# Performance work log

Measured on AMD Instinct MI355X. Metric: run time of the kernel, lower is better.

## Reference

```python
import jax, jax.numpy as jnp
import numpy as np
from jax.scipy.special import logsumexp

DIM_N, DIM_E, DIM_U = 64, 128, 64
MID, A = 32, 16
N_PER, B = 12, 128  # 128 fully-connected graphs of 12 nodes


def _lin_params(k, fin, fout):
    k1, k2 = jax.random.split(k)
    lim = 1.0 / np.sqrt(fin)
    W = jax.random.uniform(k1, (fin, fout), minval=-lim, maxval=lim)
    b = jax.random.uniform(k2, (fout,), minval=-lim, maxval=lim)
    return W, b


def setup_inputs() -> dict:
    key = jax.random.key(0)
    ks = jax.random.split(key, 12)
    # fully connected directed graph (no self loops), per component
    s, d = np.meshgrid(np.arange(N_PER), np.arange(N_PER), indexing='ij')
    m = s != d
    s1, d1 = s[m].astype(np.int64), d[m].astype(np.int64)
    Epg = s1.size  # 132
    M = np.zeros((N_PER, N_PER), np.int64)
    M[s1, d1] = np.arange(Epg)
    rev1 = M[d1, s1]
    noff = (np.arange(B, dtype=np.int64) * N_PER)[:, None]
    eoff = (np.arange(B, dtype=np.int64) * Epg)[:, None]
    src = jnp.asarray((s1[None] + noff).reshape(-1))
    dst = jnp.asarray((d1[None] + noff).reshape(-1))
    idx_revs = jnp.asarray((rev1[None] + eoff).reshape(-1))
    E, Nt = B * Epg, B * N_PER
    edge_feats = jax.random.normal(ks[0], (E, DIM_E))
    node_feats = jax.random.normal(ks[1], (Nt, DIM_N))
    graph_feats = jax.random.normal(ks[2], (B, DIM_U))
    edge_feat_reflected = edge_feats[idx_revs]
    u = jax.random.uniform(ks[3], (E, 2), minval=1e-6, maxval=1.0)
    gumbel_noise = -jnp.log(-jnp.log(u))
    W_jf, b_jf = _lin_params(ks[4], DIM_E + DIM_U, A * MID)
    W_if, b_if = _lin_params(ks[5], DIM_N + DIM_U, A)
    W_ju, b_ju = _lin_params(ks[6], DIM_E + DIM_U, A * MID)
    W_iu, b_iu = _lin_params(ks[7], DIM_N + DIM_U, A)
    W_fl, b_fl = _lin_params(ks[8], DIM_E + DIM_U, MID)
    W_cls, b_cls = _lin_params(ks[9], MID, 2)
    return dict(edge_feats=edge_feats, node_feats=node_feats, graph_feats=graph_feats,
                edge_feat_reflected=edge_feat_reflected, src=src, dst=dst, idx_revs=idx_revs,
                gumbel_noise=gumbel_noise, W_jf=W_jf, b_jf=b_jf, W_if=W_if, b_if=b_if,
                W_ju=W_ju, b_ju=b_ju, W_iu=W_iu, b_iu=b_iu, W_fl=W_fl, b_fl=b_fl,
                W_cls=W_cls, b_cls=b_cls)


def reference(edge_feats, node_feats, graph_feats, edge_feat_reflected, src, dst, idx_revs,
              gumbel_noise, W_jf, b_jf, W_if, b_if, W_ju, b_ju, W_iu, b_iu,
              W_fl, b_fl, W_cls, b_cls):
    Bn = graph_feats.shape[0]
    Nt = node_feats.shape[0]
    E = edge_feats.shape[0]
    npg = Nt // Bn          # nodes per graph == number of BP iterations
    epg = E // Bn
    a = b_if.shape[0]       # num_acts
    mid = W_cls.shape[0]    # mid_pair

    # broadcast graph-level features to edges / nodes
    u_e = jnp.repeat(graph_feats, epg, axis=0)   # [E, du]
    u_n = jnp.repeat(graph_feats, npg, axis=0)   # [Nt, du]

    xe = jnp.concatenate([edge_feats, u_e], axis=-1)
    xer = jnp.concatenate([edge_feat_reflected, u_e], axis=-1)
    xn = jnp.concatenate([node_feats, u_n], axis=-1)

    indiv_factor = xn @ W_if + b_if      # [Nt, A]
    indiv_util = xn @ W_iu + b_iu        # [Nt, A]

    fc = (xe @ W_jf + b_jf).reshape(E, a, mid)
    fcr = (xer @ W_jf + b_jf).reshape(E, a, mid)
    factor_vals = jnp.einsum('eam,ebm->eab', fc, fcr)   # [E, A, A]
    uc = (xe @ W_ju + b_ju).reshape(E, a, mid)
    ucr = (xer @ W_ju + b_ju).reshape(E, a, mid)
    util_vals = jnp.einsum('eam,ebm->eab', uc, ucr)     # [E, A, A]

    # hard gumbel-softmax edge gating; noise shared with reverse edge
    flag_repr = (xe @ W_fl + b_fl) * (xer @ W_fl + b_fl)
    logits = flag_repr @ W_cls + b_cls                  # [E, 2]
    eid = jnp.arange(E)
    noise = gumbel_noise[jnp.minimum(eid, idx_revs)]
    y_soft = jax.nn.softmax(logits + noise, axis=-1)
    y_hard = jax.nn.one_hot(jnp.argmax(y_soft, axis=-1), 2, dtype=y_soft.dtype)
    flags = y_soft + jax.lax.stop_gradient(y_hard - y_soft)
    flag0 = flags[:, 0][:, None]                        # [E, 1]

    fvT = factor_vals.transpose(0, 2, 1)
    uvT = util_vals.transpose(0, 2, 1)
    if_src, if_dst = indiv_factor[src], indiv_factor[dst]
    iu_src, iu_dst = indiv_util[src], indiv_util[dst]

    def step(carry, _):
        mm_n, um_n, msg_e, rmsg_e, umsg_e, rumsg_e = carry
        agg = mm_n[src] - rmsg_e + if_src                      # [E, A]
        m = factor_vals + agg[:, None, :]                      # [E, A, A]
        m_sum = jax.nn.log_softmax(logsumexp(m, axis=-1), axis=-1)
        new_msg = m_sum * flag0
        agg_rev = mm_n[dst] - msg_e + if_dst
        m_rev = fvT + agg_rev[:, None, :]
        m_rev_sum = jax.nn.log_softmax(logsumexp(m_rev, axis=-1), axis=-1)
        new_rmsg = m_rev_sum * flag0
        util = um_n[src] - rumsg_e + iu_src
        new_umsg = ((util_vals + util[:, None, :]) * jax.nn.softmax(m, axis=-1)).sum(-1) * flag0
        rev_util = um_n[dst] - umsg_e + iu_dst
        new_rumsg = ((uvT + rev_util[:, None, :]) * jax.nn.softmax(m_rev, axis=-1)).sum(-1) * flag0
        new_mm_n = jax.ops.segment_sum(new_msg, dst, num_segments=Nt)
        new_um_n = jax.ops.segment_sum(new_umsg, dst, num_segments=Nt)
        return (new_mm_n, new_um_n, new_msg, new_rmsg, new_umsg, new_rumsg), None

    zn = jnp.zeros((Nt, a), edge_feats.dtype)
    ze = jnp.zeros((E, a), edge_feats.dtype)
    carry0 = (zn, zn, ze, ze, ze, ze)
    (mm_n, um_n, _, _, _, _), _ = jax.lax.scan(step, carry0, None, length=npg)

    node0 = jnp.arange(Bn) * npg
    return (um_n + indiv_util)[node0]   # [B, A]
```

## Files before the change

kernel.cpp:

```cpp
#include <hip/hip_runtime.h>
#include <hip/hip_bf16.h>

typedef unsigned short ushort_t;
typedef __bf16 bf16x8 __attribute__((ext_vector_type(8)));
typedef float f32x4 __attribute__((ext_vector_type(4)));

#define E_TOT 16896
#define NT    1536
#define BGR   128
#define NPG   12
#define EPG   132
#define KD    192
#define KD2   576
#define NJ    512
#define ADIM  16
#define MIDD  32
#define NCAN  8448

#if defined(__has_builtin)
#  if __has_builtin(__builtin_amdgcn_global_load_lds)
#    define HAS_GLL 1
#  else
#    define HAS_GLL 0
#  endif
#else
#  define HAS_GLL 0
#endif

#if HAS_GLL
__device__ __forceinline__ void gll16(const ushort_t* g, ushort_t* s) {
    __builtin_amdgcn_global_load_lds(
        (const __attribute__((address_space(1))) unsigned int*)g,
        (__attribute__((address_space(3))) unsigned int*)s, 16, 0, 0);
}
#endif

__device__ __forceinline__ float b2f(ushort_t u) {
    union { float f; unsigned int i; } c; c.i = ((unsigned int)u) << 16; return c.f;
}
__device__ __forceinline__ ushort_t f2b(float f) {
    union { float f; unsigned int i; } c; c.f = f;
    unsigned int i = c.i;
    unsigned int r = (i + 0x7FFFu + ((i >> 16) & 1u)) >> 16;
    return (ushort_t)r;
}
__device__ __forceinline__ int rev_local(int i) {
    int s = i / 11;
    int p = i - 11 * s;
    int d = p + (p >= s ? 1 : 0);
    return d * 11 + (s < d ? s : s - 1);
}

__global__ __launch_bounds__(256) void prep_kernel(
    const float* __restrict__ Wjf, const float* __restrict__ Wju,
    const float* __restrict__ ef,  const float* __restrict__ gf,
    ushort_t* __restrict__ WtJFs, ushort_t* __restrict__ WtJUs,
    ushort_t* __restrict__ XeS)
{
    int idx = blockIdx.x * 256 + threadIdx.x;
    const int T1 = NJ * KD;
    if (idx < T1) {
        int n = idx / KD, k = idx - n * KD;
        float wf = Wjf[k * NJ + n];
        ushort_t hf = f2b(wf);
        WtJFs[n * KD2 + k]       = hf;
        WtJFs[n * KD2 + 192 + k] = hf;
        WtJFs[n * KD2 + 384 + k] = f2b(wf - b2f(hf));
        float wu = Wju[k * NJ + n];
        ushort_t hu = f2b(wu);
        WtJUs[n * KD2 + k]       = hu;
        WtJUs[n * KD2 + 192 + k] = hu;
        WtJUs[n * KD2 + 384 + k] = f2b(wu - b2f(hu));
        return;
    }
    idx -= T1;
    if (idx < E_TOT * KD) {
        int e = idx / KD, k = idx - e * KD;
        float x = (k < 128) ? ef[(size_t)e * 128 + k] : gf[(e / EPG) * 64 + (k - 128)];
        ushort_t h = f2b(x);
        XeS[(size_t)e * KD2 + k]       = h;
        XeS[(size_t)e * KD2 + 192 + k] = f2b(x - b2f(h));
        XeS[(size_t)e * KD2 + 384 + k] = h;
    }
}

__global__ __launch_bounds__(256) void gemm_kernel(
    const ushort_t* __restrict__ X,
    const ushort_t* __restrict__ Wt0, const ushort_t* __restrict__ Wt1,
    const float* __restrict__ b0, const float* __restrict__ b1,
    float* __restrict__ Hbase)
{
    __shared__ ushort_t As[2][128][32];
    __shared__ ushort_t Bs[2][128][32];
    int z = blockIdx.z;
    const ushort_t* Wt = z ? Wt1 : Wt0;
    const float* bias = z ? b1 : b0;
    float* H = Hbase + (size_t)z * E_TOT * NJ;

    int tid = threadIdx.x, lane = tid & 63, w = tid >> 6;
    int m0 = blockIdx.y * 128, n0 = blockIdx.x * 128;
    int wm = (w >> 1) * 64, wn = (w & 1) * 64;
    int r = lane & 15, q = lane >> 4;
    f32x4 acc[4][4] = {};

    int sr = w * 32 + (lane >> 2);
    int sc = (lane & 3) * 8;
    const ushort_t* xg0 = X  + (size_t)(m0 + sr)      * KD2 + sc;
    const ushort_t* xg1 = X  + (size_t)(m0 + sr + 16) * KD2 + sc;
    const ushort_t* wg0 = Wt + (size_t)(n0 + sr)      * KD2 + sc;
    const ushort_t* wg1 = Wt + (size_t)(n0 + sr + 16) * KD2 + sc;

#if HAS_GLL
    auto stage = [&](int p, int kk) {
        gll16(xg0 + kk, &As[p][w * 32][0]);
        gll16(xg1 + kk, &As[p][w * 32 + 16][0]);
        gll16(wg0 + kk, &Bs[p][w * 32][0]);
        gll16(wg1 + kk, &Bs[p][w * 32 + 16][0]);
    };
#else
    auto stage = [&](int p, int kk) {
        uint4 a0 = *(const uint4*)(xg0 + kk);
        uint4 a1 = *(const uint4*)(xg1 + kk);
        uint4 bb0 = *(const uint4*)(wg0 + kk);
        uint4 bb1 = *(const uint4*)(wg1 + kk);
        *(uint4*)&As[p][sr][sc]      = a0;
        *(uint4*)&As[p][sr + 16][sc] = a1;
        *(uint4*)&Bs[p][sr][sc]      = bb0;
        *(uint4*)&Bs[p][sr + 16][sc] = bb1;
    };
#endif

    stage(0, 0);
    int cur = 0;
    for (int kk = 0; kk < KD2; kk += 32) {
        __syncthreads();
        if (kk + 32 < KD2) stage(cur ^ 1, kk + 32);
        bf16x8 af[4], bf[4];
#pragma unroll
        for (int mi = 0; mi < 4; ++mi)
            af[mi] = *(const bf16x8*)&As[cur][wm + mi * 16 + r][q * 8];
#pragma unroll
        for (int ni = 0; ni < 4; ++ni)
            bf[ni] = *(const bf16x8*)&Bs[cur][wn + ni * 16 + r][q * 8];
#pragma unroll
        for (int mi = 0; mi < 4; ++mi)
#pragma unroll
            for (int ni = 0; ni < 4; ++ni)
                acc[mi][ni] = __builtin_amdgcn_mfma_f32_16x16x32_bf16(
                    af[mi], bf[ni], acc[mi][ni], 0, 0, 0);
        cur ^= 1;
    }
#pragma unroll
    for (int ni = 0; ni < 4; ++ni) {
        int col = n0 + wn + ni * 16 + r;
        float bvf = bias[col];
#pragma unroll
        for (int mi = 0; mi < 4; ++mi) {
            int rowb = m0 + wm + mi * 16 + q * 4;
            float* dst = H + (size_t)rowb * NJ + col;
#pragma unroll
            for (int rr = 0; rr < 4; ++rr)
                dst[(size_t)rr * NJ] = acc[mi][ni][rr] + bvf;
        }
    }
}

__global__ __launch_bounds__(256) void pair_kernel(
    const float* __restrict__ Hbase, float* __restrict__ Obase)
{
    __shared__ float sA[4][16][36];
    __shared__ float sB[4][16][36];
    __shared__ float sC[4][16][20];
    const float* H = Hbase + (size_t)blockIdx.y * E_TOT * NJ;
    float* OutV = Obase + (size_t)blockIdx.y * E_TOT * 256;
    int tid = threadIdx.x, w = tid >> 6, lane = tid & 63;
    int c = blockIdx.x * 4 + w;
    int gg = c / 66, cl = c - gg * 66;
    int s = 0;
    while (cl >= 11 - s) { cl -= 11 - s; ++s; }
    int d = s + 1 + cl;
    int e  = gg * EPG + s * 11 + (d - 1);
    int re = gg * EPG + d * 11 + s;
    const float* hA = H + (size_t)e * NJ;
    const float* hB = H + (size_t)re * NJ;
    int a = lane >> 2, mseg = (lane & 3) * 8;
    float4 va0 = *(const float4*)(hA + a * 32 + mseg);
    float4 va1 = *(const float4*)(hA + a * 32 + mseg + 4);
    float4 vb0 = *(const float4*)(hB + a * 32 + mseg);
    float4 vb1 = *(const float4*)(hB + a * 32 + mseg + 4);
    *(float4*)&sA[w][a][mseg]     = va0;
    *(float4*)&sA[w][a][mseg + 4] = va1;
    *(float4*)&sB[w][a][mseg]     = vb0;
    *(float4*)&sB[w][a][mseg + 4] = vb1;
    __syncthreads();

    int b = lane & 15, a0 = (lane >> 4) * 4;
    float4 ac0 = {0,0,0,0}, ac1 = {0,0,0,0}, ac2 = {0,0,0,0}, ac3 = {0,0,0,0};
#pragma unroll
    for (int m4 = 0; m4 < 8; ++m4) {
        float4 vb = *(const float4*)&sB[w][b][m4 * 4];
        float4 x0 = *(const float4*)&sA[w][a0 + 0][m4 * 4];
        float4 x1 = *(const float4*)&sA[w][a0 + 1][m4 * 4];
        float4 x2 = *(const float4*)&sA[w][a0 + 2][m4 * 4];
        float4 x3 = *(const float4*)&sA[w][a0 + 3][m4 * 4];
        ac0.x += x0.x * vb.x; ac0.y += x0.y * vb.y; ac0.z += x0.z * vb.z; ac0.w += x0.w * vb.w;
        ac1.x += x1.x * vb.x; ac1.y += x1.y * vb.y; ac1.z += x1.z * vb.z; ac1.w += x1.w * vb.w;
        ac2.x += x2.x * vb.x; ac2.y += x2.y * vb.y; ac2.z += x2.z * vb.z; ac2.w += x2.w * vb.w;
        ac3.x += x3.x * vb.x; ac3.y += x3.y * vb.y; ac3.z += x3.z * vb.z; ac3.w += x3.w * vb.w;
    }
    float v0 = ac0.x + ac0.y + ac0.z + ac0.w;
    float v1 = ac1.x + ac1.y + ac1.z + ac1.w;
    float v2 = ac2.x + ac2.y + ac2.z + ac2.w;
    float v3 = ac3.x + ac3.y + ac3.z + ac3.w;
    float* oe = OutV + (size_t)e * 256;
    oe[(a0 + 0) * 16 + b] = v0;
    oe[(a0 + 1) * 16 + b] = v1;
    oe[(a0 + 2) * 16 + b] = v2;
    oe[(a0 + 3) * 16 + b] = v3;
    sC[w][b][a0 + 0] = v0;
    sC[w][b][a0 + 1] = v1;
    sC[w][b][a0 + 2] = v2;
    sC[w][b][a0 + 3] = v3;
    __syncthreads();
    int rr = lane >> 2, cc = (lane & 3) * 4;
    float4 t4 = { sC[w][rr][cc], sC[w][rr][cc + 1], sC[w][rr][cc + 2], sC[w][rr][cc + 3] };
    *(float4*)(OutV + (size_t)re * 256 + lane * 4) = t4;
}

__global__ __launch_bounds__(256) void hfl_kernel(
    const float* __restrict__ ef, const float* __restrict__ gf,
    const float* __restrict__ Wfl, const float* __restrict__ bfl,
    float* __restrict__ HFL)
{
    __shared__ float Ws[KD][32];
    __shared__ float xr[64][KD];
    int tid = threadIdx.x;
    int e0 = blockIdx.x * 64;
    for (int i = tid; i < KD * 32; i += 256) Ws[i >> 5][i & 31] = Wfl[i];
    for (int i4 = tid; i4 < 64 * 48; i4 += 256) {
        int slot = i4 / 48, kq = i4 - slot * 48;
        int e = e0 + slot;
        float4 v;
        if (kq < 32) v = *(const float4*)&ef[(size_t)e * 128 + kq * 4];
        else         v = *(const float4*)&gf[(e / EPG) * 64 + (kq - 32) * 4];
        *(float4*)&xr[slot][kq * 4] = v;
    }
    __syncthreads();
    int j = tid & 31, es = tid >> 5;
    float acc[8];
#pragma unroll
    for (int i = 0; i < 8; ++i) acc[i] = bfl[j];
    for (int k = 0; k < KD; k += 4) {
        float w0 = Ws[k][j], w1 = Ws[k + 1][j], w2 = Ws[k + 2][j], w3 = Ws[k + 3][j];
#pragma unroll
        for (int i = 0; i < 8; ++i) {
            float4 x4 = *(const float4*)&xr[es + 8 * i][k];
            acc[i] += x4.x * w0; acc[i] += x4.y * w1;
            acc[i] += x4.z * w2; acc[i] += x4.w * w3;
        }
    }
#pragma unroll
    for (int i = 0; i < 8; ++i)
        HFL[(size_t)(e0 + es + 8 * i) * 32 + j] = acc[i];
}

__global__ __launch_bounds__(704, 3) void bp_kernel(
    const float* __restrict__ FV, const float* __restrict__ UV,
    const float* __restrict__ HFL, const float* __restrict__ Wcls,
    const float* __restrict__ bcls, const float* __restrict__ gum,
    const float* __restrict__ nf, const float* __restrict__ gf,
    const float* __restrict__ Wif, const float* __restrict__ bif,
    const float* __restrict__ Wiu, const float* __restrict__ biu,
    float* __restrict__ out)
{
    int g = blockIdx.x, tid = threadIdx.x;
    __shared__ float msg[2][EPG][16];
    __shared__ float umsg[2][EPG][16];
    __shared__ float Asum[NPG][16], Usum[NPG][16];
    __shared__ float iffs[NPG][16], iuus[NPG][16];
    __shared__ float fls[EPG];

    for (int i = tid; i < 2 * EPG * 16; i += 704) {
        (&msg[0][0][0])[i] = 0.f;
        (&umsg[0][0][0])[i] = 0.f;
    }
    if (tid < NPG * 16) {
        int nl = tid >> 4, aa = tid & 15;
        int n = g * NPG + nl;
        float accf = bif[aa], accu = biu[aa];
        for (int k = 0; k < 128; ++k) {
            float x = (k < 64) ? nf[(size_t)n * 64 + k] : gf[g * 64 + (k - 64)];
            accf += x * Wif[k * 16 + aa];
            accu += x * Wiu[k * 16 + aa];
        }
        iffs[nl][aa] = accf; iuus[nl][aa] = accu;
        Asum[nl][aa] = accf; Usum[nl][aa] = accu;
    }
    if (tid < EPG) {
        int el = tid, rel = rev_local(el);
        int e = g * EPG + el, re = g * EPG + rel;
        float l0 = bcls[0], l1 = bcls[1];
        const float* ha = HFL + (size_t)e * 32;
        const float* hb = HFL + (size_t)re * 32;
#pragma unroll
        for (int j = 0; j < 32; ++j) {
            float p = ha[j] * hb[j];
            l0 += p * Wcls[j * 2 + 0];
            l1 += p * Wcls[j * 2 + 1];
        }
        int mn = min(e, re);
        l0 += gum[(size_t)mn * 2 + 0];
        l1 += gum[(size_t)mn * 2 + 1];
        fls[el] = (l0 >= l1) ? 1.0f : 0.0f;
    }

    int w44 = tid >> 4, a = tid & 15;
    int sidx[3], ridx[3], eidx[3];
    float fv[3][16], uv[3][16], fle[3];
    const float* fvg = FV + (size_t)g * EPG * 256;
    const float* uvg = UV + (size_t)g * EPG * 256;
#pragma unroll
    for (int j = 0; j < 3; ++j) {
        int e = j * 44 + w44;
        eidx[j] = e;
        sidx[j] = e / 11;
        ridx[j] = rev_local(e);
        const float* fr = fvg + (size_t)e * 256 + a * 16;
        const float* ur = uvg + (size_t)e * 256 + a * 16;
#pragma unroll
        for (int q = 0; q < 4; ++q) {
            float4 f4 = *(const float4*)(fr + q * 4);
            float4 u4 = *(const float4*)(ur + q * 4);
            fv[j][q * 4 + 0] = f4.x; fv[j][q * 4 + 1] = f4.y;
            fv[j][q * 4 + 2] = f4.z; fv[j][q * 4 + 3] = f4.w;
            uv[j][q * 4 + 0] = u4.x; uv[j][q * 4 + 1] = u4.y;
            uv[j][q * 4 + 2] = u4.z; uv[j][q * 4 + 3] = u4.w;
        }
    }
    __syncthreads();
#pragma unroll
    for (int j = 0; j < 3; ++j) fle[j] = fls[eidx[j]];

    int cur = 0;
    for (int it = 0; it < NPG; ++it) {
        int nxt = cur ^ 1;
#pragma unroll
        for (int j = 0; j < 3; ++j) {
            int e = eidx[j], s = sidx[j], re = ridx[j];
            float t_m[16], t_u[16];
#pragma unroll
            for (int q = 0; q < 4; ++q) {
                float4 av  = *(const float4*)&Asum[s][q * 4];
                float4 mv  = *(const float4*)&msg[cur][re][q * 4];
                float4 usv = *(const float4*)&Usum[s][q * 4];
                float4 umv = *(const float4*)&umsg[cur][re][q * 4];
                t_m[q * 4 + 0] = fv[j][q * 4 + 0] + (av.x - mv.x);
                t_m[q * 4 + 1] = fv[j][q * 4 + 1] + (av.y - mv.y);
                t_m[q * 4 + 2] = fv[j][q * 4 + 2] + (av.z - mv.z);
                t_m[q * 4 + 3] = fv[j][q * 4 + 3] + (av.w - mv.w);
                t_u[q * 4 + 0] = uv[j][q * 4 + 0] + (usv.x - umv.x);
                t_u[q * 4 + 1] = uv[j][q * 4 + 1] + (usv.y - umv.y);
                t_u[q * 4 + 2] = uv[j][q * 4 + 2] + (usv.z - umv.z);
                t_u[q * 4 + 3] = uv[j][q * 4 + 3] + (usv.w - umv.w);
            }
            float mx = t_m[0];
#pragma unroll
            for (int b = 1; b < 16; ++b) mx = fmaxf(mx, t_m[b]);
            float S = 0.f, num = 0.f;
#pragma unroll
            for (int b = 0; b < 16; ++b) {
                float ev = __expf(t_m[b] - mx);
                S += ev;
                num += t_u[b] * ev;
            }
            float lse = mx + __logf(S);
            float unv = num / S;
            float M2 = lse;
            M2 = fmaxf(M2, __shfl_xor(M2, 1));
            M2 = fmaxf(M2, __shfl_xor(M2, 2));
            M2 = fmaxf(M2, __shfl_xor(M2, 4));
            M2 = fmaxf(M2, __shfl_xor(M2, 8));
            float se = __expf(lse - M2);
            se += __shfl_xor(se, 1);
            se += __shfl_xor(se, 2);
            se += __shfl_xor(se, 4);
            se += __shfl_xor(se, 8);
            float LSE = M2 + __logf(se);
            msg[nxt][e][a] = (lse - LSE) * fle[j];
            umsg[nxt][e][a] = unv * fle[j];
        }
        __syncthreads();
        if (tid < NPG * 16) {
            int n = tid >> 4, aa = tid & 15;
            float sm = 0.f, su = 0.f;
#pragma unroll
            for (int s = 0; s < NPG; ++s) {
                if (s == n) continue;
                int le = s * 11 + (n < s ? n : n - 1);
                sm += msg[nxt][le][aa];
                su += umsg[nxt][le][aa];
            }
            Asum[n][aa] = sm + iffs[n][aa];
            Usum[n][aa] = su + iuus[n][aa];
        }
        __syncthreads();
        cur = nxt;
    }
    if (tid < 16) {
        out[g * 16 + tid] = Usum[0][tid];
    }
}

extern "C" void kernel_launch(void* const* d_in, const int* in_sizes, int n_in,
                              void* d_out, int out_size, void* d_ws, size_t ws_size,
                              hipStream_t stream) {
    const float* edge_feats  = (const float*)d_in[0];
    const float* node_feats  = (const float*)d_in[1];
    const float* graph_feats = (const float*)d_in[2];
    const float* gumbel      = (const float*)d_in[7];
    const float* W_jf        = (const float*)d_in[8];
    const float* b_jf        = (const float*)d_in[9];
    const float* W_if        = (const float*)d_in[10];
    const float* b_if        = (const float*)d_in[11];
    const float* W_ju        = (const float*)d_in[12];
    const float* b_ju        = (const float*)d_in[13];
    const float* W_iu        = (const float*)d_in[14];
    const float* b_iu        = (const float*)d_in[15];
    const float* W_fl        = (const float*)d_in[16];
    const float* b_fl        = (const float*)d_in[17];
    const float* W_cls       = (const float*)d_in[18];
    const float* b_cls       = (const float*)d_in[19];
    float* out = (float*)d_out;
    (void)in_sizes; (void)n_in; (void)out_size;

    size_t off = 0;
    char* base = (char*)d_ws;
    auto alloc = [&](size_t bytes) {
        void* p = base + off;
        off += (bytes + 255) & ~(size_t)255;
        return p;
    };
    ushort_t* XeS   = (ushort_t*)alloc((size_t)E_TOT * KD2 * 2);
    ushort_t* WtJFs = (ushort_t*)alloc((size_t)NJ * KD2 * 2);
    ushort_t* WtJUs = (ushort_t*)alloc((size_t)NJ * KD2 * 2);
    float*    HFL   = (float*)   alloc((size_t)E_TOT * 32 * 4);

    const size_t fused_need = off + (size_t)E_TOT * NJ * 2 * 4
                                  + (size_t)E_TOT * 512 * 4
                                  + 4096;
    const int prep_blocks = (NJ * KD + E_TOT * KD) / 256;

    prep_kernel<<<prep_blocks, 256, 0, stream>>>(W_jf, W_ju, edge_feats, graph_feats,
                                                 WtJFs, WtJUs, XeS);
    hfl_kernel<<<E_TOT / 64, 256, 0, stream>>>(edge_feats, graph_feats, W_fl, b_fl, HFL);

    if (ws_size >= fused_need) {
        float* H2   = (float*)alloc((size_t)E_TOT * NJ * 2 * 4);
        float* FVUV = (float*)alloc((size_t)E_TOT * 512 * 4);
        float* FVv = FVUV;
        float* UVv = FVUV + (size_t)E_TOT * 256;
        gemm_kernel<<<dim3(NJ / 128, E_TOT / 128, 2), 256, 0, stream>>>(
            XeS, WtJFs, WtJUs, b_jf, b_ju, H2);
        pair_kernel<<<dim3(NCAN / 4, 2), 256, 0, stream>>>(H2, FVUV);
        bp_kernel<<<BGR, 704, 0, stream>>>(FVv, UVv, HFL, W_cls, b_cls, gumbel,
                                           node_feats, graph_feats,
                                           W_if, b_if, W_iu, b_iu, out);
    } else {
        float* Hbuf = (float*)alloc((size_t)E_TOT * NJ * 4);
        float* FVv  = (float*)alloc((size_t)E_TOT * 256 * 4);
        float* UVv  = (float*)XeS;
        gemm_kernel<<<dim3(NJ / 128, E_TOT / 128, 1), 256, 0, stream>>>(
            XeS, WtJFs, WtJFs, b_jf, b_jf, Hbuf);
        pair_kernel<<<dim3(NCAN / 4, 1), 256, 0, stream>>>(Hbuf, FVv);
        gemm_kernel<<<dim3(NJ / 128, E_TOT / 128, 1), 256, 0, stream>>>(
            XeS, WtJUs, WtJUs, b_ju, b_ju, Hbuf);
        pair_kernel<<<dim3(NCAN / 4, 1), 256, 0, stream>>>(Hbuf, UVv);
        bp_kernel<<<BGR, 704, 0, stream>>>(FVv, UVv, HFL, W_cls, b_cls, gumbel,
                                           node_feats, graph_feats,
                                           W_if, b_if, W_iu, b_iu, out);
    }
}
```

Baseline: 240.7 us.

## Share A tile across both weight GEMMs and precompute node linears in prep

The GEMM kernel now computes both the factor and utility projections in a single block. It stages one X tile against two weight tiles and keeps two accumulator sets, so X is read from memory once instead of twice. The per-node individual factor/utility linear layers move out of the serial bp_kernel preamble into extra prep_kernel blocks that use shared-memory weights. The low-workspace fallback path is removed. Doubling the accumulators raises register and LDS pressure in the GEMM, which may lower occupancy.

```diff
diff --git a/kernel.cpp b/kernel.cpp
--- a/kernel.cpp
+++ b/kernel.cpp
@@ -13,8 +13,6 @@
 #define KD    192
 #define KD2   576
 #define NJ    512
-#define ADIM  16
-#define MIDD  32
 #define NCAN  8448
 
 #if defined(__has_builtin)
@@ -54,34 +52,61 @@
 __global__ __launch_bounds__(256) void prep_kernel(
     const float* __restrict__ Wjf, const float* __restrict__ Wju,
     const float* __restrict__ ef,  const float* __restrict__ gf,
+    const float* __restrict__ nf,
+    const float* __restrict__ Wif, const float* __restrict__ bif,
+    const float* __restrict__ Wiu, const float* __restrict__ biu,
     ushort_t* __restrict__ WtJFs, ushort_t* __restrict__ WtJUs,
-    ushort_t* __restrict__ XeS)
+    ushort_t* __restrict__ XeS,
+    float* __restrict__ IFF, float* __restrict__ IUU)
 {
-    int idx = blockIdx.x * 256 + threadIdx.x;
+    __shared__ float Ws[128 * 32];
+    __shared__ float xr[8][128];
     const int T1 = NJ * KD;
-    if (idx < T1) {
-        int n = idx / KD, k = idx - n * KD;
-        float wf = Wjf[k * NJ + n];
-        ushort_t hf = f2b(wf);
-        WtJFs[n * KD2 + k]       = hf;
-        WtJFs[n * KD2 + 192 + k] = hf;
-        WtJFs[n * KD2 + 384 + k] = f2b(wf - b2f(hf));
-        float wu = Wju[k * NJ + n];
-        ushort_t hu = f2b(wu);
-        WtJUs[n * KD2 + k]       = hu;
-        WtJUs[n * KD2 + 192 + k] = hu;
-        WtJUs[n * KD2 + 384 + k] = f2b(wu - b2f(hu));
-        return;
-    }
-    idx -= T1;
-    if (idx < E_TOT * KD) {
+    const int NBE = (T1 + E_TOT * KD) / 256;
+    if (blockIdx.x < (unsigned)NBE) {
+        int idx = blockIdx.x * 256 + threadIdx.x;
+        if (idx < T1) {
+            int n = idx / KD, k = idx - n * KD;
+            float wf = Wjf[k * NJ + n];
+            ushort_t hf = f2b(wf);
+            WtJFs[n * KD2 + k]       = hf;
+            WtJFs[n * KD2 + 192 + k] = hf;
+            WtJFs[n * KD2 + 384 + k] = f2b(wf - b2f(hf));
+            float wu = Wju[k * NJ + n];
+            ushort_t hu = f2b(wu);
+            WtJUs[n * KD2 + k]       = hu;
+            WtJUs[n * KD2 + 192 + k] = hu;
+            WtJUs[n * KD2 + 384 + k] = f2b(wu - b2f(hu));
+            return;
+        }
+        idx -= T1;
         int e = idx / KD, k = idx - e * KD;
         float x = (k < 128) ? ef[(size_t)e * 128 + k] : gf[(e / EPG) * 64 + (k - 128)];
         ushort_t h = f2b(x);
         XeS[(size_t)e * KD2 + k]       = h;
         XeS[(size_t)e * KD2 + 192 + k] = f2b(x - b2f(h));
         XeS[(size_t)e * KD2 + 384 + k] = h;
-    }
+        return;
+    }
+    int tid = threadIdx.x;
+    int n0 = (blockIdx.x - NBE) * 8;
+    for (int i = tid; i < 128 * 32; i += 256) {
+        int k = i >> 5, j = i & 31;
+        Ws[i] = (j < 16) ? Wif[k * 16 + j] : Wiu[k * 16 + (j - 16)];
+    }
+    for (int i = tid; i < 8 * 128; i += 256) {
+        int slot = i >> 7, k = i & 127;
+        int n = n0 + slot;
+        xr[slot][k] = (k < 64) ? nf[(size_t)n * 64 + k] : gf[(n / NPG) * 64 + (k - 64)];
+    }
+    __syncthreads();
+    int slot = tid >> 5, j = tid & 31;
+    float acc = (j < 16) ? bif[j] : biu[j - 16];
+#pragma unroll 8
+    for (int k = 0; k < 128; ++k) acc += xr[slot][k] * Ws[k * 32 + j];
+    int n = n0 + slot;
+    if (j < 16) IFF[n * 16 + j] = acc;
+    else        IUU[n * 16 + (j - 16)] = acc;
 }
 
 __global__ __launch_bounds__(256) void gemm_kernel(
@@ -91,42 +116,45 @@
     float* __restrict__ Hbase)
 {
     __shared__ ushort_t As[2][128][32];
-    __shared__ ushort_t Bs[2][128][32];
-    int z = blockIdx.z;
-    const ushort_t* Wt = z ? Wt1 : Wt0;
-    const float* bias = z ? b1 : b0;
-    float* H = Hbase + (size_t)z * E_TOT * NJ;
-
+    __shared__ ushort_t Bs[2][2][128][32];
     int tid = threadIdx.x, lane = tid & 63, w = tid >> 6;
     int m0 = blockIdx.y * 128, n0 = blockIdx.x * 128;
     int wm = (w >> 1) * 64, wn = (w & 1) * 64;
     int r = lane & 15, q = lane >> 4;
-    f32x4 acc[4][4] = {};
+    f32x4 acc[2][4][4] = {};
 
     int sr = w * 32 + (lane >> 2);
     int sc = (lane & 3) * 8;
-    const ushort_t* xg0 = X  + (size_t)(m0 + sr)      * KD2 + sc;
-    const ushort_t* xg1 = X  + (size_t)(m0 + sr + 16) * KD2 + sc;
-    const ushort_t* wg0 = Wt + (size_t)(n0 + sr)      * KD2 + sc;
-    const ushort_t* wg1 = Wt + (size_t)(n0 + sr + 16) * KD2 + sc;
+    const ushort_t* xg0 = X   + (size_t)(m0 + sr)      * KD2 + sc;
+    const ushort_t* xg1 = X   + (size_t)(m0 + sr + 16) * KD2 + sc;
+    const ushort_t* w0g0 = Wt0 + (size_t)(n0 + sr)      * KD2 + sc;
+    const ushort_t* w0g1 = Wt0 + (size_t)(n0 + sr + 16) * KD2 + sc;
+    const ushort_t* w1g0 = Wt1 + (size_t)(n0 + sr)      * KD2 + sc;
+    const ushort_t* w1g1 = Wt1 + (size_t)(n0 + sr + 16) * KD2 + sc;
 
 #if HAS_GLL
     auto stage = [&](int p, int kk) {
-        gll16(xg0 + kk, &As[p][w * 32][0]);
-        gll16(xg1 + kk, &As[p][w * 32 + 16][0]);
-        gll16(wg0 + kk, &Bs[p][w * 32][0]);
-        gll16(wg1 + kk, &Bs[p][w * 32 + 16][0]);
+        gll16(xg0 + kk,  &As[p][w * 32][0]);
+        gll16(xg1 + kk,  &As[p][w * 32 + 16][0]);
+        gll16(w0g0 + kk, &Bs[p][0][w * 32][0]);
+        gll16(w0g1 + kk, &Bs[p][0][w * 32 + 16][0]);
+        gll16(w1g0 + kk, &Bs[p][1][w * 32][0]);
+        gll16(w1g1 + kk, &Bs[p][1][w * 32 + 16][0]);
     };
 #else
     auto stage = [&](int p, int kk) {
         uint4 a0 = *(const uint4*)(xg0 + kk);
         uint4 a1 = *(const uint4*)(xg1 + kk);
-        uint4 bb0 = *(const uint4*)(wg0 + kk);
-        uint4 bb1 = *(const uint4*)(wg1 + kk);
-        *(uint4*)&As[p][sr][sc]      = a0;
-        *(uint4*)&As[p][sr + 16][sc] = a1;
-        *(uint4*)&Bs[p][sr][sc]      = bb0;
-        *(uint4*)&Bs[p][sr + 16][sc] = bb1;
+        uint4 c0 = *(const uint4*)(w0g0 + kk);
+        uint4 c1 = *(const uint4*)(w0g1 + kk);
+        uint4 d0 = *(const uint4*)(w1g0 + kk);
+        uint4 d1 = *(const uint4*)(w1g1 + kk);
+        *(uint4*)&As[p][sr][sc]         = a0;
+        *(uint4*)&As[p][sr + 16][sc]    = a1;
+        *(uint4*)&Bs[p][0][sr][sc]      = c0;
+        *(uint4*)&Bs[p][0][sr + 16][sc] = c1;
+        *(uint4*)&Bs[p][1][sr][sc]      = d0;
+        *(uint4*)&Bs[p][1][sr + 16][sc] = d1;
     };
 #endif
 
@@ -135,32 +163,41 @@
     for (int kk = 0; kk < KD2; kk += 32) {
         __syncthreads();
         if (kk + 32 < KD2) stage(cur ^ 1, kk + 32);
-        bf16x8 af[4], bf[4];
+        bf16x8 af[4];
 #pragma unroll
         for (int mi = 0; mi < 4; ++mi)
             af[mi] = *(const bf16x8*)&As[cur][wm + mi * 16 + r][q * 8];
 #pragma unroll
-        for (int ni = 0; ni < 4; ++ni)
-            bf[ni] = *(const bf16x8*)&Bs[cur][wn + ni * 16 + r][q * 8];
-#pragma unroll
-        for (int mi = 0; mi < 4; ++mi)
+        for (int z = 0; z < 2; ++z) {
+            bf16x8 bf[4];
 #pragma unroll
             for (int ni = 0; ni < 4; ++ni)
-                acc[mi][ni] = __builtin_amdgcn_mfma_f32_16x16x32_bf16(
-                    af[mi], bf[ni], acc[mi][ni], 0, 0, 0);
+                bf[ni] = *(const bf16x8*)&Bs[cur][z][wn + ni * 16 + r][q * 8];
+#pragma unroll
+            for (int mi = 0; mi < 4; ++mi)
+#pragma unroll
+                for (int ni = 0; ni < 4; ++ni)
+                    acc[z][mi][ni] = __builtin_amdgcn_mfma_f32_16x16x32_bf16(
+                        af[mi], bf[ni], acc[z][mi][ni], 0, 0, 0);
+        }
         cur ^= 1;
     }
 #pragma unroll
-    for (int ni = 0; ni < 4; ++ni) {
-        int col = n0 + wn + ni * 16 + r;
-        float bvf = bias[col];
-#pragma unroll
-        for (int mi = 0; mi < 4; ++mi) {
-            int rowb = m0 + wm + mi * 16 + q * 4;
-            float* dst = H + (size_t)rowb * NJ + col;
-#pragma unroll
-            for (int rr = 0; rr < 4; ++rr)
-                dst[(size_t)rr * NJ] = acc[mi][ni][rr] + bvf;
+    for (int z = 0; z < 2; ++z) {
+        float* H = Hbase + (size_t)z * E_TOT * NJ;
+        const float* bias = z ? b1 : b0;
+#pragma unroll
+        for (int ni = 0; ni < 4; ++ni) {
+            int col = n0 + wn + ni * 16 + r;
+            float bvf = bias[col];
+#pragma unroll
+            for (int mi = 0; mi < 4; ++mi) {
+                int rowb = m0 + wm + mi * 16 + q * 4;
+                float* dst = H + (size_t)rowb * NJ + col;
+#pragma unroll
+                for (int rr = 0; rr < 4; ++rr)
+                    dst[(size_t)rr * NJ] = acc[z][mi][ni][rr] + bvf;
+            }
         }
     }
 }
@@ -268,9 +305,7 @@
     const float* __restrict__ FV, const float* __restrict__ UV,
     const float* __restrict__ HFL, const float* __restrict__ Wcls,
     const float* __restrict__ bcls, const float* __restrict__ gum,
-    const float* __restrict__ nf, const float* __restrict__ gf,
-    const float* __restrict__ Wif, const float* __restrict__ bif,
-    const float* __restrict__ Wiu, const float* __restrict__ biu,
+    const float* __restrict__ IFF, const float* __restrict__ IUU,
     float* __restrict__ out)
 {
     int g = blockIdx.x, tid = threadIdx.x;
@@ -285,16 +320,10 @@
         (&umsg[0][0][0])[i] = 0.f;
     }
     if (tid < NPG * 16) {
-        int nl = tid >> 4, aa = tid & 15;
-        int n = g * NPG + nl;
-        float accf = bif[aa], accu = biu[aa];
-        for (int k = 0; k < 128; ++k) {
-            float x = (k < 64) ? nf[(size_t)n * 64 + k] : gf[g * 64 + (k - 64)];
-            accf += x * Wif[k * 16 + aa];
-            accu += x * Wiu[k * 16 + aa];
-        }
-        iffs[nl][aa] = accf; iuus[nl][aa] = accu;
-        Asum[nl][aa] = accf; Usum[nl][aa] = accu;
+        float fi = IFF[g * NPG * 16 + tid];
+        float ui = IUU[g * NPG * 16 + tid];
+        (&iffs[0][0])[tid] = fi; (&iuus[0][0])[tid] = ui;
+        (&Asum[0][0])[tid] = fi; (&Usum[0][0])[tid] = ui;
     }
     if (tid < EPG) {
         int el = tid, rel = rev_local(el);
@@ -304,9 +333,9 @@
         const float* hb = HFL + (size_t)re * 32;
 #pragma unroll
         for (int j = 0; j < 32; ++j) {
-            float p = ha[j] * hb[j];
-            l0 += p * Wcls[j * 2 + 0];
-            l1 += p * Wcls[j * 2 + 1];
+            float pp = ha[j] * hb[j];
+            l0 += pp * Wcls[j * 2 + 0];
+            l1 += pp * Wcls[j * 2 + 1];
         }
         int mn = min(e, re);
         l0 += gum[(size_t)mn * 2 + 0];
@@ -328,13 +357,13 @@
         const float* fr = fvg + (size_t)e * 256 + a * 16;
         const float* ur = uvg + (size_t)e * 256 + a * 16;
 #pragma unroll
-        for (int q = 0; q < 4; ++q) {
-            float4 f4 = *(const float4*)(fr + q * 4);
-            float4 u4 = *(const float4*)(ur + q * 4);
-            fv[j][q * 4 + 0] = f4.x; fv[j][q * 4 + 1] = f4.y;
-            fv[j][q * 4 + 2] = f4.z; fv[j][q * 4 + 3] = f4.w;
-            uv[j][q * 4 + 0] = u4.x; uv[j][q * 4 + 1] = u4.y;
-            uv[j][q * 4 + 2] = u4.z; uv[j][q * 4 + 3] = u4.w;
+        for (int qq = 0; qq < 4; ++qq) {
+            float4 f4 = *(const float4*)(fr + qq * 4);
+            float4 u4 = *(const float4*)(ur + qq * 4);
+            fv[j][qq * 4 + 0] = f4.x; fv[j][qq * 4 + 1] = f4.y;
+            fv[j][qq * 4 + 2] = f4.z; fv[j][qq * 4 + 3] = f4.w;
+            uv[j][qq * 4 + 0] = u4.x; uv[j][qq * 4 + 1] = u4.y;
+            uv[j][qq * 4 + 2] = u4.z; uv[j][qq * 4 + 3] = u4.w;
         }
     }
     __syncthreads();
@@ -349,19 +378,19 @@
             int e = eidx[j], s = sidx[j], re = ridx[j];
             float t_m[16], t_u[16];
 #pragma unroll
-            for (int q = 0; q < 4; ++q) {
-                float4 av  = *(const float4*)&Asum[s][q * 4];
-                float4 mv  = *(const float4*)&msg[cur][re][q * 4];
-                float4 usv = *(const float4*)&Usum[s][q * 4];
-                float4 umv = *(const float4*)&umsg[cur][re][q * 4];
-                t_m[q * 4 + 0] = fv[j][q * 4 + 0] + (av.x - mv.x);
-                t_m[q * 4 + 1] = fv[j][q * 4 + 1] + (av.y - mv.y);
-                t_m[q * 4 + 2] = fv[j][q * 4 + 2] + (av.z - mv.z);
-                t_m[q * 4 + 3] = fv[j][q * 4 + 3] + (av.w - mv.w);
-                t_u[q * 4 + 0] = uv[j][q * 4 + 0] + (usv.x - umv.x);
-                t_u[q * 4 + 1] = uv[j][q * 4 + 1] + (usv.y - umv.y);
-                t_u[q * 4 + 2] = uv[j][q * 4 + 2] + (usv.z - umv.z);
-                t_u[q * 4 + 3] = uv[j][q * 4 + 3] + (usv.w - umv.w);
+            for (int qq = 0; qq < 4; ++qq) {
+                float4 av  = *(const float4*)&Asum[s][qq * 4];
+                float4 mv  = *(const float4*)&msg[cur][re][qq * 4];
+                float4 usv = *(const float4*)&Usum[s][qq * 4];
+                float4 umv = *(const float4*)&umsg[cur][re][qq * 4];
+                t_m[qq * 4 + 0] = fv[j][qq * 4 + 0] + (av.x - mv.x);
+                t_m[qq * 4 + 1] = fv[j][qq * 4 + 1] + (av.y - mv.y);
+                t_m[qq * 4 + 2] = fv[j][qq * 4 + 2] + (av.z - mv.z);
+                t_m[qq * 4 + 3] = fv[j][qq * 4 + 3] + (av.w - mv.w);
+                t_u[qq * 4 + 0] = uv[j][qq * 4 + 0] + (usv.x - umv.x);
+                t_u[qq * 4 + 1] = uv[j][qq * 4 + 1] + (usv.y - umv.y);
+                t_u[qq * 4 + 2] = uv[j][qq * 4 + 2] + (usv.z - umv.z);
+                t_u[qq * 4 + 3] = uv[j][qq * 4 + 3] + (usv.w - umv.w);
             }
             float mx = t_m[0];
 #pragma unroll
@@ -431,7 +460,7 @@
     const float* W_cls       = (const float*)d_in[18];
     const float* b_cls       = (const float*)d_in[19];
     float* out = (float*)d_out;
-    (void)in_sizes; (void)n_in; (void)out_size;
+    (void)in_sizes; (void)n_in; (void)out_size; (void)ws_size;
 
     size_t off = 0;
     char* base = (char*)d_ws;
@@ -444,39 +473,23 @@
     ushort_t* WtJFs = (ushort_t*)alloc((size_t)NJ * KD2 * 2);
     ushort_t* WtJUs = (ushort_t*)alloc((size_t)NJ * KD2 * 2);
     float*    HFL   = (float*)   alloc((size_t)E_TOT * 32 * 4);
-
-    const size_t fused_need = off + (size_t)E_TOT * NJ * 2 * 4
-                                  + (size_t)E_TOT * 512 * 4
-                                  + 4096;
-    const int prep_blocks = (NJ * KD + E_TOT * KD) / 256;
-
-    prep_kernel<<<prep_blocks, 256, 0, stream>>>(W_jf, W_ju, edge_feats, graph_feats,
-                                                 WtJFs, WtJUs, XeS);
+    float*    IFFp  = (float*)   alloc((size_t)NT * 16 * 4);
+    float*    IUUp  = (float*)   alloc((size_t)NT * 16 * 4);
+    float*    H2    = (float*)   alloc((size_t)E_TOT * NJ * 2 * 4);
+    float*    FVUV  = (float*)   alloc((size_t)E_TOT * 512 * 4);
+    float* FVv = FVUV;
+    float* UVv = FVUV + (size_t)E_TOT * 256;
+
+    const int NBE = (NJ * KD + E_TOT * KD) / 256;
+    const int prep_blocks = NBE + NT / 8;
+
+    prep_kernel<<<prep_blocks, 256, 0, stream>>>(
+        W_jf, W_ju, edge_feats, graph_feats, node_feats,
+        W_if, b_if, W_iu, b_iu, WtJFs, WtJUs, XeS, IFFp, IUUp);
     hfl_kernel<<<E_TOT / 64, 256, 0, stream>>>(edge_feats, graph_feats, W_fl, b_fl, HFL);
-
-    if (ws_size >= fused_need) {
-        float* H2   = (float*)alloc((size_t)E_TOT * NJ * 2 * 4);
-        float* FVUV = (float*)alloc((size_t)E_TOT * 512 * 4);
-        float* FVv = FVUV;
-        float* UVv = FVUV + (size_t)E_TOT * 256;
-        gemm_kernel<<<dim3(NJ / 128, E_TOT / 128, 2), 256, 0, stream>>>(
-            XeS, WtJFs, WtJUs, b_jf, b_ju, H2);
-        pair_kernel<<<dim3(NCAN / 4, 2), 256, 0, stream>>>(H2, FVUV);
-        bp_kernel<<<BGR, 704, 0, stream>>>(FVv, UVv, HFL, W_cls, b_cls, gumbel,
-                                           node_feats, graph_feats,
-                                           W_if, b_if, W_iu, b_iu, out);
-    } else {
-        float* Hbuf = (float*)alloc((size_t)E_TOT * NJ * 4);
-        float* FVv  = (float*)alloc((size_t)E_TOT * 256 * 4);
-        float* UVv  = (float*)XeS;
-        gemm_kernel<<<dim3(NJ / 128, E_TOT / 128, 1), 256, 0, stream>>>(
-            XeS, WtJFs, WtJFs, b_jf, b_jf, Hbuf);
-        pair_kernel<<<dim3(NCAN / 4, 1), 256, 0, stream>>>(Hbuf, FVv);
-        gemm_kernel<<<dim3(NJ / 128, E_TOT / 128, 1), 256, 0, stream>>>(
-            XeS, WtJUs, WtJUs, b_ju, b_ju, Hbuf);
-        pair_kernel<<<dim3(NCAN / 4, 1), 256, 0, stream>>>(Hbuf, UVv);
-        bp_kernel<<<BGR, 704, 0, stream>>>(FVv, UVv, HFL, W_cls, b_cls, gumbel,
-                                           node_feats, graph_feats,
-                                           W_if, b_if, W_iu, b_iu, out);
-    }
-}
+    gemm_kernel<<<dim3(NJ / 128, E_TOT / 128), 256, 0, stream>>>(
+        XeS, WtJFs, WtJUs, b_jf, b_ju, H2);
+    pair_kernel<<<dim3(NCAN / 4, 2), 256, 0, stream>>>(H2, FVUV);
+    bp_kernel<<<BGR, 704, 0, stream>>>(FVv, UVv, HFL, W_cls, b_cls, gumbel,
+                                       IFFp, IUUp, out);
+}
```

After: 241.5 us. No clear change (+0.3%).
